# Kernel optimization log

Measured on AMD Instinct MI355X. Metric: run time of the kernel, lower is better.

Reference implementation:

```python
import jax, jax.numpy as jnp
import numpy as np

N = 20000      # nodes
E = 320000     # edges (before self-loops)
F_IN = 512     # input feature size
HID = 128      # encoder hidden
OUT = 128      # encoder output / GAT in_channels
H = 4          # gat heads
C = 64         # gat out_channels per head


def setup_inputs() -> dict:
    key = jax.random.key(0)
    ks = jax.random.split(key, 10)
    s = 0.05
    return {
        "x": jax.random.normal(ks[0], (N, F_IN), jnp.float32),
        "edge_index": jax.random.randint(ks[1], (2, E), 0, N, dtype=jnp.int64),
        "W1": jax.random.normal(ks[2], (F_IN, HID), jnp.float32) * s,
        "b1": jax.random.normal(ks[3], (HID,), jnp.float32) * s,
        "W2": jax.random.normal(ks[4], (HID, OUT), jnp.float32) * s,
        "b2": jax.random.normal(ks[5], (OUT,), jnp.float32) * s,
        "Wg": jax.random.normal(ks[6], (OUT, H * C), jnp.float32) * s,
        "att_src": jax.random.normal(ks[7], (H, C), jnp.float32) * s,
        "att_dst": jax.random.normal(ks[8], (H, C), jnp.float32) * s,
        "bias_g": jax.random.normal(ks[9], (H * C,), jnp.float32) * s,
    }


def reference(x, edge_index, W1, b1, W2, b2, Wg, att_src, att_dst, bias_g):
    # MLP encoder: Linear -> ReLU -> Linear
    h = jnp.maximum(x @ W1 + b1, 0.0) @ W2 + b2            # [N, OUT]

    # GATConv (concat=True, eval mode -> no dropout)
    xg = (h @ Wg).reshape(N, H, C)                          # per-head projections

    # add self-loops (PyG GATConv default)
    loops = jnp.arange(N, dtype=edge_index.dtype)
    src = jnp.concatenate([edge_index[0], loops])           # [E+N] source j
    dst = jnp.concatenate([edge_index[1], loops])           # [E+N] dest   i

    a_src = jnp.einsum('nhc,hc->nh', xg, att_src)           # [N, H]
    a_dst = jnp.einsum('nhc,hc->nh', xg, att_dst)           # [N, H]

    e = jax.nn.leaky_relu(a_src[src] + a_dst[dst], 0.2)     # [E+N, H]

    # segment softmax over incoming edges of each destination node
    m = jax.ops.segment_max(e, dst, num_segments=N)         # [N, H]
    ex = jnp.exp(e - m[dst])
    denom = jax.ops.segment_sum(ex, dst, num_segments=N)
    alpha = ex / (denom[dst] + 1e-16)                       # [E+N, H]

    # weighted scatter-add aggregation
    out = jax.ops.segment_sum(alpha[:, :, None] * xg[src], dst, num_segments=N)  # [N, H, C]
    return out.reshape(N, H * C) + bias_g
```

## Files before the change

kernel.cpp:

```cpp
#include <hip/hip_runtime.h>
#include <math.h>

#define NNODES 20000
#define NEDGES 320000
#define FIN    512
#define HIDD   128
#define OUTD   128
#define NH     4
#define NC     64
#define HC     256

typedef short bf16x8 __attribute__((ext_vector_type(8)));
typedef float f32x4  __attribute__((ext_vector_type(4)));

__device__ __forceinline__ unsigned short f2bf(float f) {
    unsigned int u = __float_as_uint(f);
    unsigned int r = 0x7fffu + ((u >> 16) & 1u);
    return (unsigned short)((u + r) >> 16);
}
__device__ __forceinline__ float b2f(short t) {
    return __uint_as_float(((unsigned)(unsigned short)t) << 16);
}
__device__ __forceinline__ float4 f4max(float4 a, float4 b) {
    return make_float4(fmaxf(a.x,b.x), fmaxf(a.y,b.y), fmaxf(a.z,b.z), fmaxf(a.w,b.w));
}
__device__ __forceinline__ float4 f4add(float4 a, float4 b) {
    return make_float4(a.x+b.x, a.y+b.y, a.z+b.z, a.w+b.w);
}
__device__ __forceinline__ float4 f4sub(float4 a, float4 b) {
    return make_float4(a.x-b.x, a.y-b.y, a.z-b.z, a.w-b.w);
}
__device__ __forceinline__ float4 f4mul(float4 a, float4 b) {
    return make_float4(a.x*b.x, a.y*b.y, a.z*b.z, a.w*b.w);
}
__device__ __forceinline__ float4 f4exp(float4 a) {
    return make_float4(__expf(a.x), __expf(a.y), __expf(a.z), __expf(a.w));
}
__device__ __forceinline__ float4 shflx4(float4 v, int m) {
    return make_float4(__shfl_xor(v.x,m), __shfl_xor(v.y,m), __shfl_xor(v.z,m), __shfl_xor(v.w,m));
}

#define PREP_TB1 64
#define PREP_TB2 192
__global__ __launch_bounds__(256)
void prep_kernel(const float* __restrict__ W1, unsigned short* __restrict__ W1t,
                 const float* __restrict__ W2, const float* __restrict__ b2,
                 const float* __restrict__ Wg, unsigned short* __restrict__ W2gt,
                 float* __restrict__ b2g, int* __restrict__ deg, int n) {
    const int bid = blockIdx.x;
    const int tid = threadIdx.x;
    if (bid < PREP_TB1) {
        __shared__ float tile[32][33];
        const int tk = bid >> 2;
        const int tn = bid & 3;
        const int k0 = tk * 32, n0 = tn * 32;
        const int nin = tid & 31;
        const int r8  = tid >> 5;
        #pragma unroll
        for (int s = 0; s < 4; ++s) {
            int k = s * 8 + r8;
            tile[k][nin] = W1[(size_t)(k0 + k) * HIDD + n0 + nin];
        }
        __syncthreads();
        #pragma unroll
        for (int s = 0; s < 4; ++s) {
            int nn = s * 8 + r8;
            W1t[(size_t)(n0 + nn) * FIN + k0 + nin] = f2bf(tile[nin][nn]);
        }
    } else if (bid < PREP_TB2) {
        int local = (bid - PREP_TB1) * 256 + tid;
        int nn = local >> 7;
        int k  = local & 127;
        float s = 0.f;
        #pragma unroll 8
        for (int t = 0; t < HIDD; ++t)
            s += W2[(size_t)k * OUTD + t] * Wg[(size_t)t * HC + nn];
        W2gt[(size_t)nn * HIDD + k] = f2bf(s);
        if (k == 0) {
            float t2 = 0.f;
            #pragma unroll 8
            for (int t = 0; t < OUTD; ++t) t2 += b2[t] * Wg[(size_t)t * HC + nn];
            b2g[nn] = t2;
        }
    } else {
        int i = (bid - PREP_TB2) * 256 + tid;
        if (i < n) deg[i] = 1;
    }
}

__global__ __launch_bounds__(256)
void gemm1_count_kernel(const float* __restrict__ A,
                        const unsigned short* __restrict__ Bt,
                        const float* __restrict__ bias,
                        unsigned short* __restrict__ C,
                        const int* __restrict__ dst, int* __restrict__ deg,
                        int M, int E, int gemmBlocks) {
    __shared__ unsigned short As[32 * 64];
    __shared__ unsigned short Bs[128 * 64];

    if ((int)blockIdx.x >= gemmBlocks) {
        int i = ((int)blockIdx.x - gemmBlocks) * 256 + threadIdx.x;
        if (i < E) atomicAdd(&deg[dst[i]], 1);
        return;
    }

    const int tid  = threadIdx.x;
    const int lane = tid & 63;
    const int w    = tid >> 6;
    const int wr   = w >> 1;
    const int wc   = w & 1;
    const int m0   = blockIdx.x * 32;

    char* pA = (char*)As;
    char* pB = (char*)Bs;

    f32x4 acc[4];
    #pragma unroll
    for (int n = 0; n < 4; ++n) acc[n] = (f32x4){0.f, 0.f, 0.f, 0.f};

    for (int k0 = 0; k0 < FIN; k0 += 64) {
        {
            const int row = tid >> 3;
            const int sg  = tid & 7;
            const bool ok = (m0 + row) < M;
            const float4* Ap = (const float4*)(A + (size_t)(m0 + row) * FIN + k0 + sg * 8);
            float4 f0 = make_float4(0,0,0,0), f1 = f0;
            if (ok) { f0 = Ap[0]; f1 = Ap[1]; }
            unsigned short u[8];
            u[0]=f2bf(f0.x); u[1]=f2bf(f0.y); u[2]=f2bf(f0.z); u[3]=f2bf(f0.w);
            u[4]=f2bf(f1.x); u[5]=f2bf(f1.y); u[6]=f2bf(f1.z); u[7]=f2bf(f1.w);
            *(bf16x8*)(pA + (((row * 128 + sg * 16)) ^ ((row & 7) << 4))) = *(bf16x8*)&u[0];
        }
        #pragma unroll
        for (int i = 0; i < 4; ++i) {
            int s   = tid + i * 256;
            int col = s >> 3;
            int sg  = s & 7;
            bf16x8 v = *(const bf16x8*)(Bt + (size_t)col * FIN + k0 + sg * 8);
            *(bf16x8*)(pB + (((col * 128 + sg * 16)) ^ ((col & 7) << 4))) = v;
        }
        __syncthreads();

        #pragma unroll
        for (int ks = 0; ks < 2; ++ks) {
            const int kb = ks * 64 + ((lane >> 4) << 4);
            int row = wr * 16 + (lane & 15);
            bf16x8 a = *(const bf16x8*)(pA + ((row * 128 + kb) ^ ((row & 7) << 4)));
            bf16x8 b[4];
            #pragma unroll
            for (int n = 0; n < 4; ++n) {
                int col = wc * 64 + n * 16 + (lane & 15);
                b[n] = *(const bf16x8*)(pB + ((col * 128 + kb) ^ ((col & 7) << 4)));
            }
            #pragma unroll
            for (int n = 0; n < 4; ++n)
                acc[n] = __builtin_amdgcn_mfma_f32_16x16x32_bf16(a, b[n], acc[n], 0, 0, 0);
        }
        __syncthreads();
    }

    #pragma unroll
    for (int n = 0; n < 4; ++n) {
        const int col = wc * 64 + n * 16 + (lane & 15);
        const float bv = bias[col];
        #pragma unroll
        for (int r = 0; r < 4; ++r) {
            const int row = m0 + wr * 16 + ((lane >> 4) << 2) + r;
            if (row >= M) continue;
            float v = fmaxf(acc[n][r] + bv, 0.f);
            C[(size_t)row * HIDD + col] = f2bf(v);
        }
    }
}

__global__ __launch_bounds__(1024)
void scan_offsets_kernel(const int* __restrict__ deg, int* __restrict__ offs,
                         int* __restrict__ cursor, int* __restrict__ csr, int n) {
    __shared__ int wsum[16], wbase[16];
    const int tid = threadIdx.x, lane = tid & 63, w = tid >> 6;
    const int i0 = tid * 20;
    int loc[20];
    int s = 0;
    #pragma unroll
    for (int k = 0; k < 20; ++k) {
        int i = i0 + k;
        int v = (i < n) ? deg[i] : 0;
        loc[k] = s;
        s += v;
    }
    int incl = s;
    #pragma unroll
    for (int d = 1; d < 64; d <<= 1) {
        int t = __shfl_up(incl, d);
        if (lane >= d) incl += t;
    }
    if (lane == 63) wsum[w] = incl;
    __syncthreads();
    if (w == 0) {
        int v = (lane < 16) ? wsum[lane] : 0;
        int sc = v;
        #pragma unroll
        for (int d = 1; d < 16; d <<= 1) {
            int t = __shfl_up(sc, d);
            if (lane >= d) sc += t;
        }
        if (lane < 16) wbase[lane] = sc - v;
    }
    __syncthreads();
    const int excl = wbase[w] + incl - s;
    #pragma unroll
    for (int k = 0; k < 20; ++k) {
        int i = i0 + k;
        if (i < n) {
            int o = excl + loc[k];
            offs[i]   = o;
            cursor[i] = o + 1;
            csr[o]    = i;
        }
    }
    if (tid == 1023) offs[n] = excl + s;
}

__global__ __launch_bounds__(256)
void gemm2_dots_scatter_kernel(const unsigned short* __restrict__ Ab,
                               const unsigned short* __restrict__ Bt,
                               const float* __restrict__ b2g,
                               const float* __restrict__ att_src,
                               const float* __restrict__ att_dst,
                               unsigned short* __restrict__ xgb,
                               float* __restrict__ a_src, float* __restrict__ a_dst,
                               const int* __restrict__ e_src, const int* __restrict__ e_dst,
                               int* __restrict__ cursor, int* __restrict__ csr,
                               int M, int E, int gemmBlocks) {
    const int tid = threadIdx.x;

    if ((int)blockIdx.x >= gemmBlocks) {
        int i = ((int)blockIdx.x - gemmBlocks) * 256 + tid;
        if (i < E) {
            int s = e_src[i], d = e_dst[i];
            csr[atomicAdd(&cursor[d], 1)] = s;
        }
        return;
    }

    __shared__ unsigned short As[64 * 64];
    __shared__ unsigned short Bs[128 * 64];

    const int lane = tid & 63;
    const int w    = tid >> 6;
    const int wr   = w >> 1;
    const int wc   = w & 1;
    const int m0   = ((int)blockIdx.x >> 1) * 64;
    const int n0   = ((int)blockIdx.x & 1) * 128;

    char* pA = (char*)As;
    char* pB = (char*)Bs;

    f32x4 acc[2][4];
    #pragma unroll
    for (int m = 0; m < 2; ++m)
        #pragma unroll
        for (int n = 0; n < 4; ++n) acc[m][n] = (f32x4){0.f, 0.f, 0.f, 0.f};

    for (int k0 = 0; k0 < HIDD; k0 += 64) {
        #pragma unroll
        for (int i = 0; i < 2; ++i) {
            int s   = tid + i * 256;
            int row = s >> 3;
            int sg  = s & 7;
            bf16x8 v = {};
            if ((m0 + row) < M)
                v = *(const bf16x8*)(Ab + (size_t)(m0 + row) * HIDD + k0 + sg * 8);
            *(bf16x8*)(pA + (((row * 128 + sg * 16)) ^ ((row & 7) << 4))) = v;
        }
        #pragma unroll
        for (int i = 0; i < 4; ++i) {
            int s   = tid + i * 256;
            int col = s >> 3;
            int sg  = s & 7;
            bf16x8 v = *(const bf16x8*)(Bt + (size_t)(n0 + col) * HIDD + k0 + sg * 8);
            *(bf16x8*)(pB + (((col * 128 + sg * 16)) ^ ((col & 7) << 4))) = v;
        }
        __syncthreads();

        #pragma unroll
        for (int ks = 0; ks < 2; ++ks) {
            const int kb = ks * 64 + ((lane >> 4) << 4);
            bf16x8 a[2], b[4];
            #pragma unroll
            for (int m = 0; m < 2; ++m) {
                int row = wr * 32 + m * 16 + (lane & 15);
                a[m] = *(const bf16x8*)(pA + ((row * 128 + kb) ^ ((row & 7) << 4)));
            }
            #pragma unroll
            for (int n = 0; n < 4; ++n) {
                int col = wc * 64 + n * 16 + (lane & 15);
                b[n] = *(const bf16x8*)(pB + ((col * 128 + kb) ^ ((col & 7) << 4)));
            }
            #pragma unroll
            for (int m = 0; m < 2; ++m)
                #pragma unroll
                for (int n = 0; n < 4; ++n)
                    acc[m][n] = __builtin_amdgcn_mfma_f32_16x16x32_bf16(
                        a[m], b[n], acc[m][n], 0, 0, 0);
        }
        __syncthreads();
    }

    const int head = ((int)blockIdx.x & 1) * 2 + wc;
    const int cIn  = lane & 15;
    float ds_p[2][4], dd_p[2][4];
    #pragma unroll
    for (int m = 0; m < 2; ++m)
        #pragma unroll
        for (int r = 0; r < 4; ++r) { ds_p[m][r] = 0.f; dd_p[m][r] = 0.f; }

    #pragma unroll
    for (int n = 0; n < 4; ++n) {
        const int ch  = n * 16 + cIn;
        const int col = n0 + wc * 64 + n * 16 + cIn;
        const float bv   = b2g[col];
        const float as_c = att_src[head * NC + ch];
        const float ad_c = att_dst[head * NC + ch];
        #pragma unroll
        for (int m = 0; m < 2; ++m) {
            #pragma unroll
            for (int r = 0; r < 4; ++r) {
                const int row = m0 + wr * 32 + m * 16 + ((lane >> 4) << 2) + r;
                float v = acc[m][n][r] + bv;
                if (row < M) xgb[(size_t)row * HC + col] = f2bf(v);
                ds_p[m][r] += v * as_c;
                dd_p[m][r] += v * ad_c;
            }
        }
    }
    #pragma unroll
    for (int m = 0; m < 2; ++m) {
        #pragma unroll
        for (int r = 0; r < 4; ++r) {
            float s = ds_p[m][r], d = dd_p[m][r];
            s += __shfl_xor(s, 1); s += __shfl_xor(s, 2);
            s += __shfl_xor(s, 4); s += __shfl_xor(s, 8);
            d += __shfl_xor(d, 1); d += __shfl_xor(d, 2);
            d += __shfl_xor(d, 4); d += __shfl_xor(d, 8);
            if (cIn == 0) {
                const int row = m0 + wr * 32 + m * 16 + ((lane >> 4) << 2) + r;
                if (row < M) {
                    a_src[row * NH + head] = s;
                    a_dst[row * NH + head] = d;
                }
            }
        }
    }
}

__global__ __launch_bounds__(256)
void gat_aggregate4_kernel(const unsigned short* __restrict__ xgb,
                           const float4* __restrict__ asrc4,
                           const float4* __restrict__ adst4,
                           const int* __restrict__ offs, const int* __restrict__ csr_src,
                           const float* __restrict__ bias, float* __restrict__ out, int n) {
    __shared__ float4 exbuf[4][64];
    __shared__ int    sbuf[4][64];
    const int wv   = threadIdx.x >> 6;
    const int lane = threadIdx.x & 63;
    const int node = blockIdx.x * 4 + wv;
    if (node >= n) return;
    const int beg = offs[node], end = offs[node + 1];
    const int deg = end - beg;
    const float4 adstv = adst4[node];

    float4 m   = make_float4(-INFINITY, -INFINITY, -INFINITY, -INFINITY);
    float4 den = make_float4(0.f, 0.f, 0.f, 0.f);
    for (int c0 = 0; c0 < deg; c0 += 64) {
        int idx = beg + c0 + lane;
        bool ok = idx < end;
        int s = ok ? csr_src[idx] : 0;
        float4 e = make_float4(-INFINITY, -INFINITY, -INFINITY, -INFINITY);
        if (ok) {
            float4 a = asrc4[s];
            e = f4add(a, adstv);
            e.x = e.x > 0.f ? e.x : 0.2f * e.x;
            e.y = e.y > 0.f ? e.y : 0.2f * e.y;
            e.z = e.z > 0.f ? e.z : 0.2f * e.z;
            e.w = e.w > 0.f ? e.w : 0.2f * e.w;
        }
        float4 cm = e;
        #pragma unroll
        for (int dd = 32; dd >= 1; dd >>= 1) cm = f4max(cm, shflx4(cm, dd));
        float4 nm = f4max(m, cm);
        float4 ex = f4exp(f4sub(e, nm));
        exbuf[wv][lane] = ex;
        sbuf[wv][lane]  = s;
        float4 cs = ex;
        #pragma unroll
        for (int dd = 32; dd >= 1; dd >>= 1) cs = f4add(cs, shflx4(cs, dd));
        den = f4add(f4mul(den, f4exp(f4sub(m, nm))), cs);
        m = nm;
    }

    const int hi = lane >> 5;
    const int ll = lane & 31;
    const int h  = ll >> 3;
    const float denh = (h == 0) ? den.x : (h == 1) ? den.y : (h == 2) ? den.z : den.w;
    const float inv = 1.f / (denh + 1e-16f);

    float4 acc0 = make_float4(0.f, 0.f, 0.f, 0.f);
    float4 acc1 = make_float4(0.f, 0.f, 0.f, 0.f);
    const float* exf = (const float*)&exbuf[wv][0];

    auto do_edge = [&](int jj) {
        int s = sbuf[wv][jj];
        float wgt = exf[jj * 4 + h];
        bf16x8 v = *(const bf16x8*)(xgb + (size_t)s * HC + ll * 8);
        acc0.x += wgt * b2f(v[0]); acc0.y += wgt * b2f(v[1]);
        acc0.z += wgt * b2f(v[2]); acc0.w += wgt * b2f(v[3]);
        acc1.x += wgt * b2f(v[4]); acc1.y += wgt * b2f(v[5]);
        acc1.z += wgt * b2f(v[6]); acc1.w += wgt * b2f(v[7]);
    };

    auto run_chunk = [&](int cn) {
        int j = 0;
        for (; j + 16 <= cn; j += 16) {
            int ss[8]; float ww[8]; bf16x8 vv[8];
            #pragma unroll
            for (int t = 0; t < 8; ++t) {
                int jj = j + 2 * t + hi;
                ss[t] = sbuf[wv][jj];
                ww[t] = exf[jj * 4 + h];
            }
            #pragma unroll
            for (int t = 0; t < 8; ++t)
                vv[t] = *(const bf16x8*)(xgb + (size_t)ss[t] * HC + ll * 8);
            #pragma unroll
            for (int t = 0; t < 8; ++t) {
                acc0.x += ww[t]*b2f(vv[t][0]); acc0.y += ww[t]*b2f(vv[t][1]);
                acc0.z += ww[t]*b2f(vv[t][2]); acc0.w += ww[t]*b2f(vv[t][3]);
                acc1.x += ww[t]*b2f(vv[t][4]); acc1.y += ww[t]*b2f(vv[t][5]);
                acc1.z += ww[t]*b2f(vv[t][6]); acc1.w += ww[t]*b2f(vv[t][7]);
            }
        }
        for (; j + 8 <= cn; j += 8) {
            do_edge(j + hi);     do_edge(j + 2 + hi);
            do_edge(j + 4 + hi); do_edge(j + 6 + hi);
        }
        for (; j + 4 <= cn; j += 4) {
            do_edge(j + hi);
            do_edge(j + 2 + hi);
        }
        for (; j < cn; j += 2) {
            int jj = j + hi;
            if (jj < cn) do_edge(jj);
        }
    };

    if (deg <= 64) {
        run_chunk(deg);
    } else {
        for (int c0 = 0; c0 < deg; c0 += 64) {
            int idx = beg + c0 + lane;
            if (idx < end) {
                int s = csr_src[idx];
                float4 e = f4add(asrc4[s], adstv);
                e.x = e.x > 0.f ? e.x : 0.2f * e.x;
                e.y = e.y > 0.f ? e.y : 0.2f * e.y;
                e.z = e.z > 0.f ? e.z : 0.2f * e.z;
                e.w = e.w > 0.f ? e.w : 0.2f * e.w;
                exbuf[wv][lane] = f4exp(f4sub(e, m));
                sbuf[wv][lane]  = s;
            }
            int cn = deg - c0; if (cn > 64) cn = 64;
            run_chunk(cn);
        }
    }

    acc0.x += __shfl_xor(acc0.x, 32); acc0.y += __shfl_xor(acc0.y, 32);
    acc0.z += __shfl_xor(acc0.z, 32); acc0.w += __shfl_xor(acc0.w, 32);
    acc1.x += __shfl_xor(acc1.x, 32); acc1.y += __shfl_xor(acc1.y, 32);
    acc1.z += __shfl_xor(acc1.z, 32); acc1.w += __shfl_xor(acc1.w, 32);

    const float4* b4 = (const float4*)bias;
    float4* op = (float4*)(out + (size_t)node * HC);
    if (hi == 0) {
        float4 bv = b4[ll * 2];
        op[ll * 2] = make_float4(acc0.x * inv + bv.x, acc0.y * inv + bv.y,
                                 acc0.z * inv + bv.z, acc0.w * inv + bv.w);
    } else {
        float4 bv = b4[ll * 2 + 1];
        op[ll * 2 + 1] = make_float4(acc1.x * inv + bv.x, acc1.y * inv + bv.y,
                                     acc1.z * inv + bv.z, acc1.w * inv + bv.w);
    }
}

extern "C" void kernel_launch(void* const* d_in, const int* in_sizes, int n_in,
                              void* d_out, int out_size, void* d_ws, size_t ws_size,
                              hipStream_t stream) {
    const float* x       = (const float*)d_in[0];
    const int*   ei      = (const int*)d_in[1];
    const float* W1      = (const float*)d_in[2];
    const float* b1      = (const float*)d_in[3];
    const float* W2      = (const float*)d_in[4];
    const float* b2      = (const float*)d_in[5];
    const float* Wg      = (const float*)d_in[6];
    const float* att_src = (const float*)d_in[7];
    const float* att_dst = (const float*)d_in[8];
    const float* bias_g  = (const float*)d_in[9];

    const int Nn = in_sizes[0] / FIN;
    const int E  = in_sizes[1] / 2;
    const int* e_src = ei;
    const int* e_dst = ei + E;

    char* w = (char*)d_ws;
    auto alloc = [&](size_t bytes) { char* p = w; w += (bytes + 255) & ~(size_t)255; return p; };
    unsigned short* W1t  = (unsigned short*)alloc((size_t)OUTD * FIN * 2);
    unsigned short* W2gt = (unsigned short*)alloc((size_t)HC * HIDD * 2);
    float* b2g  = (float*)alloc(HC * 4);
    unsigned short* h1  = (unsigned short*)alloc((size_t)Nn * HIDD * 2);
    unsigned short* xgb = (unsigned short*)alloc((size_t)Nn * HC * 2);
    float* asrc = (float*)alloc((size_t)Nn * NH * 4);
    float* adst = (float*)alloc((size_t)Nn * NH * 4);
    int* deg    = (int*)alloc((size_t)Nn * 4);
    int* offs   = (int*)alloc((size_t)(Nn + 1) * 4);
    int* cursor = (int*)alloc((size_t)Nn * 4);
    int* csr    = (int*)alloc((size_t)(E + Nn) * 4);

    dim3 blk(256);

    {
        int nb = PREP_TB2 + (Nn + 255) / 256;
        prep_kernel<<<dim3(nb), blk, 0, stream>>>(
            W1, W1t, W2, b2, Wg, W2gt, b2g, deg, Nn);
    }

    {
        int gb = (Nn + 31) / 32;
        int cb = (E + 255) / 256;
        gemm1_count_kernel<<<dim3(gb + cb), blk, 0, stream>>>(
            x, W1t, b1, h1, e_dst, deg, Nn, E, gb);
    }

    scan_offsets_kernel<<<dim3(1), dim3(1024), 0, stream>>>(deg, offs, cursor, csr, Nn);

    {
        int gb = ((Nn + 63) / 64) * 2;
        int sb = (E + 255) / 256;
        gemm2_dots_scatter_kernel<<<dim3(gb + sb), blk, 0, stream>>>(
            h1, W2gt, b2g, att_src, att_dst, xgb, asrc, adst,
            e_src, e_dst, cursor, csr, Nn, E, gb);
    }

    gat_aggregate4_kernel<<<dim3((Nn + 3) / 4), blk, 0, stream>>>(
        xgb, (const float4*)asrc, (const float4*)adst, offs, csr, bias_g,
        (float*)d_out, Nn);
}
```

Measured before the change: 131.0 us.

## Store GAT features head-major and aggregate per head without online max

GEMM2 now writes the projected features as four per-head planes instead of interleaved rows. The aggregation kernel is rewritten so each wavefront handles one (node, head) pair. Eight lane groups each process edges and gather 128-byte bf16 rows from the head plane, then reduce with shuffles. The segment-max pass and LDS staging are dropped by exponentiating the raw scores directly. This removes a pass over edges and shared-memory traffic, but risks overflow for large attention logits and launches four times as many blocks. The degree-count blocks also now process four edges per thread.

```diff
diff --git a/kernel.cpp b/kernel.cpp
--- a/kernel.cpp
+++ b/kernel.cpp
@@ -20,24 +20,6 @@
 }
 __device__ __forceinline__ float b2f(short t) {
     return __uint_as_float(((unsigned)(unsigned short)t) << 16);
-}
-__device__ __forceinline__ float4 f4max(float4 a, float4 b) {
-    return make_float4(fmaxf(a.x,b.x), fmaxf(a.y,b.y), fmaxf(a.z,b.z), fmaxf(a.w,b.w));
-}
-__device__ __forceinline__ float4 f4add(float4 a, float4 b) {
-    return make_float4(a.x+b.x, a.y+b.y, a.z+b.z, a.w+b.w);
-}
-__device__ __forceinline__ float4 f4sub(float4 a, float4 b) {
-    return make_float4(a.x-b.x, a.y-b.y, a.z-b.z, a.w-b.w);
-}
-__device__ __forceinline__ float4 f4mul(float4 a, float4 b) {
-    return make_float4(a.x*b.x, a.y*b.y, a.z*b.z, a.w*b.w);
-}
-__device__ __forceinline__ float4 f4exp(float4 a) {
-    return make_float4(__expf(a.x), __expf(a.y), __expf(a.z), __expf(a.w));
-}
-__device__ __forceinline__ float4 shflx4(float4 v, int m) {
-    return make_float4(__shfl_xor(v.x,m), __shfl_xor(v.y,m), __shfl_xor(v.z,m), __shfl_xor(v.w,m));
 }
 
 #define PREP_TB1 64
@@ -99,8 +81,12 @@
     __shared__ unsigned short Bs[128 * 64];
 
     if ((int)blockIdx.x >= gemmBlocks) {
-        int i = ((int)blockIdx.x - gemmBlocks) * 256 + threadIdx.x;
-        if (i < E) atomicAdd(&deg[dst[i]], 1);
+        int base = ((int)blockIdx.x - gemmBlocks) * 1024 + threadIdx.x;
+        #pragma unroll
+        for (int t = 0; t < 4; ++t) {
+            int i = base + t * 256;
+            if (i < E) atomicAdd(&deg[dst[i]], 1);
+        }
         return;
     }
 
@@ -227,7 +213,7 @@
                                const float* __restrict__ b2g,
                                const float* __restrict__ att_src,
                                const float* __restrict__ att_dst,
-                               unsigned short* __restrict__ xgb,
+                               unsigned short* __restrict__ xgh,
                                float* __restrict__ a_src, float* __restrict__ a_dst,
                                const int* __restrict__ e_src, const int* __restrict__ e_dst,
                                int* __restrict__ cursor, int* __restrict__ csr,
@@ -309,6 +295,7 @@
 
     const int head = ((int)blockIdx.x & 1) * 2 + wc;
     const int cIn  = lane & 15;
+    unsigned short* plane = xgh + (size_t)head * M * NC;
     float ds_p[2][4], dd_p[2][4];
     #pragma unroll
     for (int m = 0; m < 2; ++m)
@@ -328,7 +315,7 @@
             for (int r = 0; r < 4; ++r) {
                 const int row = m0 + wr * 32 + m * 16 + ((lane >> 4) << 2) + r;
                 float v = acc[m][n][r] + bv;
-                if (row < M) xgb[(size_t)row * HC + col] = f2bf(v);
+                if (row < M) plane[(size_t)row * NC + ch] = f2bf(v);
                 ds_p[m][r] += v * as_c;
                 dd_p[m][r] += v * ad_c;
             }
@@ -355,140 +342,72 @@
 }
 
 __global__ __launch_bounds__(256)
-void gat_aggregate4_kernel(const unsigned short* __restrict__ xgb,
-                           const float4* __restrict__ asrc4,
-                           const float4* __restrict__ adst4,
-                           const int* __restrict__ offs, const int* __restrict__ csr_src,
-                           const float* __restrict__ bias, float* __restrict__ out, int n) {
-    __shared__ float4 exbuf[4][64];
-    __shared__ int    sbuf[4][64];
+void gat_aggregate5_kernel(const unsigned short* __restrict__ xgh,
+                           const float* __restrict__ asrc,
+                           const float* __restrict__ adst,
+                           const int* __restrict__ offs, const int* __restrict__ csr,
+                           const float* __restrict__ bias, float* __restrict__ out,
+                           int n, int nbPerHead) {
     const int wv   = threadIdx.x >> 6;
     const int lane = threadIdx.x & 63;
-    const int node = blockIdx.x * 4 + wv;
+    const int head = (int)blockIdx.x / nbPerHead;
+    const int node = ((int)blockIdx.x % nbPerHead) * 4 + wv;
     if (node >= n) return;
-    const int beg = offs[node], end = offs[node + 1];
-    const int deg = end - beg;
-    const float4 adstv = adst4[node];
-
-    float4 m   = make_float4(-INFINITY, -INFINITY, -INFINITY, -INFINITY);
-    float4 den = make_float4(0.f, 0.f, 0.f, 0.f);
-    for (int c0 = 0; c0 < deg; c0 += 64) {
-        int idx = beg + c0 + lane;
-        bool ok = idx < end;
-        int s = ok ? csr_src[idx] : 0;
-        float4 e = make_float4(-INFINITY, -INFINITY, -INFINITY, -INFINITY);
-        if (ok) {
-            float4 a = asrc4[s];
-            e = f4add(a, adstv);
-            e.x = e.x > 0.f ? e.x : 0.2f * e.x;
-            e.y = e.y > 0.f ? e.y : 0.2f * e.y;
-            e.z = e.z > 0.f ? e.z : 0.2f * e.z;
-            e.w = e.w > 0.f ? e.w : 0.2f * e.w;
-        }
-        float4 cm = e;
-        #pragma unroll
-        for (int dd = 32; dd >= 1; dd >>= 1) cm = f4max(cm, shflx4(cm, dd));
-        float4 nm = f4max(m, cm);
-        float4 ex = f4exp(f4sub(e, nm));
-        exbuf[wv][lane] = ex;
-        sbuf[wv][lane]  = s;
-        float4 cs = ex;
-        #pragma unroll
-        for (int dd = 32; dd >= 1; dd >>= 1) cs = f4add(cs, shflx4(cs, dd));
-        den = f4add(f4mul(den, f4exp(f4sub(m, nm))), cs);
-        m = nm;
-    }
-
-    const int hi = lane >> 5;
-    const int ll = lane & 31;
-    const int h  = ll >> 3;
-    const float denh = (h == 0) ? den.x : (h == 1) ? den.y : (h == 2) ? den.z : den.w;
-    const float inv = 1.f / (denh + 1e-16f);
-
-    float4 acc0 = make_float4(0.f, 0.f, 0.f, 0.f);
-    float4 acc1 = make_float4(0.f, 0.f, 0.f, 0.f);
-    const float* exf = (const float*)&exbuf[wv][0];
-
-    auto do_edge = [&](int jj) {
-        int s = sbuf[wv][jj];
-        float wgt = exf[jj * 4 + h];
-        bf16x8 v = *(const bf16x8*)(xgb + (size_t)s * HC + ll * 8);
-        acc0.x += wgt * b2f(v[0]); acc0.y += wgt * b2f(v[1]);
-        acc0.z += wgt * b2f(v[2]); acc0.w += wgt * b2f(v[3]);
-        acc1.x += wgt * b2f(v[4]); acc1.y += wgt * b2f(v[5]);
-        acc1.z += wgt * b2f(v[6]); acc1.w += wgt * b2f(v[7]);
-    };
-
-    auto run_chunk = [&](int cn) {
-        int j = 0;
-        for (; j + 16 <= cn; j += 16) {
-            int ss[8]; float ww[8]; bf16x8 vv[8];
-            #pragma unroll
-            for (int t = 0; t < 8; ++t) {
-                int jj = j + 2 * t + hi;
-                ss[t] = sbuf[wv][jj];
-                ww[t] = exf[jj * 4 + h];
-            }
-            #pragma unroll
-            for (int t = 0; t < 8; ++t)
-                vv[t] = *(const bf16x8*)(xgb + (size_t)ss[t] * HC + ll * 8);
-            #pragma unroll
-            for (int t = 0; t < 8; ++t) {
-                acc0.x += ww[t]*b2f(vv[t][0]); acc0.y += ww[t]*b2f(vv[t][1]);
-                acc0.z += ww[t]*b2f(vv[t][2]); acc0.w += ww[t]*b2f(vv[t][3]);
-                acc1.x += ww[t]*b2f(vv[t][4]); acc1.y += ww[t]*b2f(vv[t][5]);
-                acc1.z += ww[t]*b2f(vv[t][6]); acc1.w += ww[t]*b2f(vv[t][7]);
-            }
-        }
-        for (; j + 8 <= cn; j += 8) {
-            do_edge(j + hi);     do_edge(j + 2 + hi);
-            do_edge(j + 4 + hi); do_edge(j + 6 + hi);
-        }
-        for (; j + 4 <= cn; j += 4) {
-            do_edge(j + hi);
-            do_edge(j + 2 + hi);
-        }
-        for (; j < cn; j += 2) {
-            int jj = j + hi;
-            if (jj < cn) do_edge(jj);
-        }
-    };
-
-    if (deg <= 64) {
-        run_chunk(deg);
-    } else {
-        for (int c0 = 0; c0 < deg; c0 += 64) {
-            int idx = beg + c0 + lane;
-            if (idx < end) {
-                int s = csr_src[idx];
-                float4 e = f4add(asrc4[s], adstv);
-                e.x = e.x > 0.f ? e.x : 0.2f * e.x;
-                e.y = e.y > 0.f ? e.y : 0.2f * e.y;
-                e.z = e.z > 0.f ? e.z : 0.2f * e.z;
-                e.w = e.w > 0.f ? e.w : 0.2f * e.w;
-                exbuf[wv][lane] = f4exp(f4sub(e, m));
-                sbuf[wv][lane]  = s;
-            }
-            int cn = deg - c0; if (cn > 64) cn = 64;
-            run_chunk(cn);
-        }
-    }
-
-    acc0.x += __shfl_xor(acc0.x, 32); acc0.y += __shfl_xor(acc0.y, 32);
-    acc0.z += __shfl_xor(acc0.z, 32); acc0.w += __shfl_xor(acc0.w, 32);
-    acc1.x += __shfl_xor(acc1.x, 32); acc1.y += __shfl_xor(acc1.y, 32);
-    acc1.z += __shfl_xor(acc1.z, 32); acc1.w += __shfl_xor(acc1.w, 32);
-
-    const float4* b4 = (const float4*)bias;
-    float4* op = (float4*)(out + (size_t)node * HC);
-    if (hi == 0) {
-        float4 bv = b4[ll * 2];
-        op[ll * 2] = make_float4(acc0.x * inv + bv.x, acc0.y * inv + bv.y,
-                                 acc0.z * inv + bv.z, acc0.w * inv + bv.w);
-    } else {
-        float4 bv = b4[ll * 2 + 1];
-        op[ll * 2 + 1] = make_float4(acc1.x * inv + bv.x, acc1.y * inv + bv.y,
-                                     acc1.z * inv + bv.z, acc1.w * inv + bv.w);
+    const int g = lane >> 3;
+    const int q = lane & 7;
+    const int beg = offs[node];
+    const int deg = offs[node + 1] - beg;
+    const float adh = adst[node * NH + head];
+    const unsigned short* plane = xgh + (size_t)head * n * NC;
+
+    float acc[8] = {0.f, 0.f, 0.f, 0.f, 0.f, 0.f, 0.f, 0.f};
+    float den = 0.f;
+
+    for (int j0 = 0; j0 < deg; j0 += 16) {
+        const int jA = j0 + g, jB = j0 + 8 + g;
+        const bool okA = jA < deg, okB = jB < deg;
+        float wA = 0.f, wB = 0.f;
+        bf16x8 vA = {}, vB = {};
+        if (okA) {
+            int s = csr[beg + jA];
+            float e = asrc[s * NH + head] + adh;
+            e = e > 0.f ? e : 0.2f * e;
+            wA = __expf(e);
+            vA = *(const bf16x8*)(plane + (size_t)s * NC + q * 8);
+        }
+        if (okB) {
+            int s = csr[beg + jB];
+            float e = asrc[s * NH + head] + adh;
+            e = e > 0.f ? e : 0.2f * e;
+            wB = __expf(e);
+            vB = *(const bf16x8*)(plane + (size_t)s * NC + q * 8);
+        }
+        den += wA + wB;
+        #pragma unroll
+        for (int t = 0; t < 8; ++t)
+            acc[t] += wA * b2f(vA[t]) + wB * b2f(vB[t]);
+    }
+
+    #pragma unroll
+    for (int mask = 8; mask <= 32; mask <<= 1) {
+        den += __shfl_xor(den, mask);
+        #pragma unroll
+        for (int t = 0; t < 8; ++t) acc[t] += __shfl_xor(acc[t], mask);
+    }
+
+    if (g == 0) {
+        const float inv = 1.f / (den + 1e-16f);
+        const int base = node * HC + head * NC + q * 8;
+        float4 o0 = make_float4(acc[0] * inv + bias[head * NC + q * 8 + 0],
+                                acc[1] * inv + bias[head * NC + q * 8 + 1],
+                                acc[2] * inv + bias[head * NC + q * 8 + 2],
+                                acc[3] * inv + bias[head * NC + q * 8 + 3]);
+        float4 o1 = make_float4(acc[4] * inv + bias[head * NC + q * 8 + 4],
+                                acc[5] * inv + bias[head * NC + q * 8 + 5],
+                                acc[6] * inv + bias[head * NC + q * 8 + 6],
+                                acc[7] * inv + bias[head * NC + q * 8 + 7]);
+        *(float4*)(out + base)     = o0;
+        *(float4*)(out + base + 4) = o1;
     }
 }
 
@@ -517,7 +436,7 @@
     unsigned short* W2gt = (unsigned short*)alloc((size_t)HC * HIDD * 2);
     float* b2g  = (float*)alloc(HC * 4);
     unsigned short* h1  = (unsigned short*)alloc((size_t)Nn * HIDD * 2);
-    unsigned short* xgb = (unsigned short*)alloc((size_t)Nn * HC * 2);
+    unsigned short* xgh = (unsigned short*)alloc((size_t)NH * Nn * NC * 2);
     float* asrc = (float*)alloc((size_t)Nn * NH * 4);
     float* adst = (float*)alloc((size_t)Nn * NH * 4);
     int* deg    = (int*)alloc((size_t)Nn * 4);
@@ -535,7 +454,7 @@
 
     {
         int gb = (Nn + 31) / 32;
-        int cb = (E + 255) / 256;
+        int cb = (E + 1023) / 1024;
         gemm1_count_kernel<<<dim3(gb + cb), blk, 0, stream>>>(
             x, W1t, b1, h1, e_dst, deg, Nn, E, gb);
     }
@@ -546,11 +465,13 @@
         int gb = ((Nn + 63) / 64) * 2;
         int sb = (E + 255) / 256;
         gemm2_dots_scatter_kernel<<<dim3(gb + sb), blk, 0, stream>>>(
-            h1, W2gt, b2g, att_src, att_dst, xgb, asrc, adst,
+            h1, W2gt, b2g, att_src, att_dst, xgh, asrc, adst,
             e_src, e_dst, cursor, csr, Nn, E, gb);
     }
 
-    gat_aggregate4_kernel<<<dim3((Nn + 3) / 4), blk, 0, stream>>>(
-        xgb, (const float4*)asrc, (const float4*)adst, offs, csr, bias_g,
-        (float*)d_out, Nn);
-}
+    {
+        int nbPerHead = (Nn + 3) / 4;
+        gat_aggregate5_kernel<<<dim3(NH * nbPerHead), blk, 0, stream>>>(
+            xgh, asrc, adst, offs, csr, bias_g, (float*)d_out, Nn, nbPerHead);
+    }
+}
```

Result: slower. 136.7 us (+4.4%).
